# Kernel optimization log

Measured on AMD Instinct MI355X. Metric: run time of the kernel, lower is better.

## Reference

```python
import jax, jax.numpy as jnp
import numpy as np

PERIOD = 24
NUM_ITERATIONS = 2


def _window_size():
    w = max(3, PERIOD // 2)  # 12
    if w % 2 == 0:
        w += 1  # 13
    return w


def moving_average(s, w):
    # s: [N, L]; replicate-pad by w//2 on each side, then width-w mean conv ('VALID')
    pad = w // 2
    sp = jnp.pad(s, ((0, 0), (pad, pad)), mode='edge')[:, None, :]  # [N,1,L+2*pad]
    k = jnp.ones((1, 1, w), s.dtype) / w
    y = jax.lax.conv_general_dilated(sp, k, window_strides=(1,), padding='VALID',
                                     dimension_numbers=('NCH', 'OIH', 'NCH'))
    return y[:, 0, :]  # [N, L]


def extract_seasonal(d):
    # d: [N, L] with L a multiple of PERIOD. Strided indices i, i+P, ... correspond
    # to reshape [N, C, P] with fixed last axis; median over cycles, broadcast back.
    N, L = d.shape
    C = L // PERIOD
    sub = d.reshape(N, C, PERIOD)
    med = jnp.median(sub, axis=1)  # [N, P] (C=121 is odd -> matches torch.median)
    return jnp.broadcast_to(med[:, None, :], (N, C, PERIOD)).reshape(N, L)


def setup_inputs() -> dict:
    key = jax.random.key(0)
    x = jax.random.normal(key, (64, 2904, 207), dtype=jnp.float32)
    return {"x": x}


def reference(x):
    # x: [B, L, F] -> process all features at once as [B*F, L]
    B, L, F = x.shape
    s = jnp.transpose(x, (0, 2, 1)).reshape(B * F, L)
    w = _window_size()
    trend = moving_average(s, w)
    for _ in range(NUM_ITERATIONS):
        seasonal = extract_seasonal(s - trend)
        trend = moving_average(s - seasonal, w)
    residual = s - trend - seasonal

    def unflatten(a):
        return jnp.transpose(a.reshape(B, F, L), (0, 2, 1))  # [B, L, F]

    return unflatten(trend), unflatten(seasonal), unflatten(residual)
```

## Files before the change

### kernel.cpp

```cpp
#include <hip/hip_runtime.h>

#define LROW    2904
#define PERIOD  24
#define CYC     121
#define NF      207
#define NB      64
#define NROWS   13248
#define FCH     8
#define NCH     26
#define KPADW   9
#define KLDS    (PERIOD * 61 * KPADW)
#define NT      256
#define LTILE   24
#define NLT     121
#define K2GRID  (NB * NLT)
#define K2CHUNK (K2GRID / 8)
#define R13     (1.f / 13.f)

typedef unsigned short us2 __attribute__((ext_vector_type(2)));

__device__ __forceinline__ int clampi(int i) {
    return i < 0 ? 0 : (i >= LROW ? LROW - 1 : i);
}
__device__ __forceinline__ unsigned quantk(float d) {
    int ki = (int)fmaf(d, 4096.f, 32768.f);
    ki = ki < 0 ? 0 : (ki > 65535 ? 65535 : ki);
    return (unsigned)ki;
}
__device__ __forceinline__ float dqmid(unsigned k) {
    return ((float)(int)k - 32767.5f) * (1.f / 4096.f);
}

__device__ __forceinline__ unsigned selN_split(const unsigned (&K)[31], int thr) {
    unsigned T = 0;
    const us2 one2 = __builtin_bit_cast(us2, 0x00010001u);
    for (int bit = 15; bit >= 0; --bit) {
        unsigned Tp = T | (1u << bit);
        unsigned tm32 = (Tp - 1u) | ((Tp - 1u) << 16);
        us2 tm2 = __builtin_bit_cast(us2, tm32);
        us2 acc = __builtin_bit_cast(us2, 0u);
        #pragma unroll
        for (int s = 0; s < 31; ++s) {
            us2 kv = __builtin_bit_cast(us2, K[s]);
            us2 dd = __builtin_elementwise_sub_sat(kv, tm2);
            us2 mm = __builtin_elementwise_min(dd, one2);
            acc = acc + mm;
        }
        unsigned a = __builtin_bit_cast(unsigned, acc);
        int cnt = (int)(a & 0xFFFFu) + (int)(a >> 16);
        cnt += __shfl_xor(cnt, 1);
        if (cnt >= thr) T = Tp;
    }
    return T;
}

__device__ __forceinline__ void loadK31(const unsigned* keyl, int p, int f,
                                        int half, unsigned (&K)[31]) {
    const int base = p * 61 * KPADW + f;
    if (!half) {
        #pragma unroll
        for (int s = 0; s < 31; ++s) K[s] = keyl[base + s * KPADW];
    } else {
        #pragma unroll
        for (int s = 0; s < 30; ++s) K[s] = keyl[base + (31 + s) * KPADW];
        K[30] = 0u;
    }
}

__global__ __launch_bounds__(256) void k_median(const float* __restrict__ x,
                                                float* __restrict__ wsTab) {
    __shared__ unsigned keyl[KLDS];
    __shared__ unsigned short m0s[PERIOD * FCH];
    __shared__ float medBs[12 * FCH];

    const int d   = blockIdx.x;
    const int blk = (d & 7) * 208 + (d >> 3);
    const int b   = blk & 63;
    const int ch  = blk >> 6;
    const int f0  = ch * FCH;
    const int t   = threadIdx.x;

    for (int i = t; i < KLDS; i += NT) keyl[i] = 0xFFFFFFFFu;
    __syncthreads();

    {
        const int f   = t & 7;
        const int seg = t >> 3;
        const int fe  = (f0 + f < NF) ? (f0 + f) : (NF - 1);
        const float* xb = x + (size_t)b * (LROW * NF) + fe;
        const int l0 = seg * 91;
        int c = l0 / PERIOD;
        int p = l0 - c * PERIOD;
        unsigned short* k16 = (unsigned short*)keyl;

        float r[13];
        float sum = 0.f;
        #pragma unroll
        for (int i = 0; i < 13; ++i) {
            int li = l0 - 7 + i; if (li < 0) li = 0;
            r[i] = xb[(size_t)li * NF];
            sum += r[i];
        }
        #pragma unroll 13
        for (int j = 0; j < 91; ++j) {
            const int l = l0 + j;
            int la = l + 6; if (la > LROW - 1) la = LROW - 1;
            float xn = xb[(size_t)la * NF];
            sum += xn - r[0];
            unsigned k = quantk(r[7] - sum * R13);
            if (l < LROW) {
                int idx = (p * 61 + (c >> 1)) * KPADW + f;
                k16[idx * 2 + (c & 1)] = (unsigned short)k;
            }
            #pragma unroll
            for (int i = 0; i < 12; ++i) r[i] = r[i + 1];
            r[12] = xn;
            ++p; if (p == PERIOD) { p = 0; ++c; }
        }
    }
    __syncthreads();

    {
        const int sel = t >> 1, half = t & 1;
        const int f = sel & 7, p = sel >> 3;
        unsigned K[31]; loadK31(keyl, p, f, half, K);
        unsigned T = selN_split(K, 62);
        if (!half) m0s[p * FCH + f] = (unsigned short)T;
    }
    if (t < 128) {
        const int sel = t >> 1, half = t & 1;
        const int f = sel & 7, p = 16 + (sel >> 3);
        unsigned K[31]; loadK31(keyl, p, f, half, K);
        unsigned T = selN_split(K, 62);
        if (!half) m0s[p * FCH + f] = (unsigned short)T;
    }
    __syncthreads();

    if (t < 192) {
        const int sel = t >> 1, half = t & 1;
        const int f = sel & 7, e = sel >> 3;
        const int p = (e < 6) ? e : e + 12;

        float m0[PERIOD];
        #pragma unroll
        for (int q = 0; q < PERIOD; ++q)
            m0[q] = dqmid(m0s[q * FCH + f]);

        float wph = 0.f, we = 0.f;
        #pragma unroll
        for (int ee = 0; ee < 12; ++ee) if (ee == e) {
            const int pp = (ee < 6) ? ee : ee + 12;
            #pragma unroll
            for (int q = 0; q < 13; ++q) wph += m0[(pp + 18 + q) % 24];
            #pragma unroll
            for (int q = -6; q <= 6; ++q) {
                int aa = pp + q; if (aa < 0) aa = 0; if (aa > 23) aa = 23;
                we += m0[aa];
            }
        }

        unsigned K[31]; loadK31(keyl, p, f, half, K);
        unsigned m = (unsigned)m0s[p * FCH + f];
        unsigned xk = ((unsigned short*)keyl)
                      [((p * 61 + (p < 6 ? 0 : 60)) * KPADW + f) * 2];
        unsigned y = quantk(dqmid(xk) + (we - wph) * R13);

        int thr = (y > m) ? 61 : 63;
        unsigned v = selN_split(K, thr);
        bool up = (y > m) && (xk <= m);
        bool dn = (y < m) && (xk >= m);
        unsigned nm = up ? (y < v ? y : v) : (dn ? (y > v ? y : v) : m);
        if (!half) medBs[e * FCH + f] = dqmid(nm) + wph * R13;
    }
    __syncthreads();

    if (t < FCH && f0 + t < NF) {
        const int f = t;
        float m0[PERIOD];
        #pragma unroll
        for (int q = 0; q < PERIOD; ++q)
            m0[q] = dqmid(m0s[q * FCH + f]);
        float W0[PERIOD];
        {
            float s = 0.f;
            #pragma unroll
            for (int q = 0; q < 13; ++q) s += m0[q];
            W0[0] = s;
            #pragma unroll
            for (int q = 1; q < PERIOD; ++q)
                W0[q] = W0[q - 1] + m0[(q + 12) % 24] - m0[q - 1];
        }
        float lm[PERIOD];
        #pragma unroll
        for (int e = 0; e < 12; ++e) {
            int p = (e < 6) ? e : e + 12;
            lm[p] = medBs[e * FCH + f];
        }
        #pragma unroll
        for (int p = 6; p < 18; ++p) lm[p] = m0[p] + W0[p - 6] * R13;
        float wt[PERIOD];
        {
            float s = 0.f;
            #pragma unroll
            for (int q = 0; q < 13; ++q) s += lm[q];
            wt[0] = s;
            #pragma unroll
            for (int q = 1; q < PERIOD; ++q)
                wt[q] = wt[q - 1] + lm[(q + 12) % 24] - lm[q - 1];
        }
        float* wrow = wsTab + (size_t)b * 48 * NF + (f0 + f);
        #pragma unroll
        for (int i = 0; i < PERIOD; ++i) {
            wrow[(size_t)i * NF]        = lm[i];
            wrow[(size_t)(24 + i) * NF] = wt[i];
        }
    }
}

__global__ __launch_bounds__(NT, 5) void stl_outputs(const float* __restrict__ x,
                                                     const float* __restrict__ ws,
                                                     float* __restrict__ out) {
    __shared__ float T[(LTILE + 12) * NF];

    const int d   = blockIdx.x;
    const int blk = (d & 7) * K2CHUNK + (d >> 3);
    const int b  = blk / NLT;
    const int kk = blk - b * NLT;
    const int l0 = kk * LTILE;
    const int t  = threadIdx.x;
    const float* xb = x + (size_t)b * (LROW * NF);

    if (kk != 0 && kk != NLT - 1) {
        const float2* s2 = (const float2*)(xb + (size_t)(l0 - 6) * NF);
        float2* t2 = (float2*)T;
        for (int i = t; i < (LTILE + 12) * NF / 2; i += NT) t2[i] = s2[i];
    } else {
        for (int i = t; i < (LTILE + 12) * NF; i += NT) {
            int lr = i / NF;
            int ff = i - lr * NF;
            T[i] = xb[(size_t)clampi(l0 - 6 + lr) * NF + ff];
        }
    }
    __syncthreads();

    if (t < NF) {
        float lm[PERIOD], wt[PERIOD];
        const float* wrow = ws + (size_t)b * 48 * NF + t;
        #pragma unroll
        for (int i = 0; i < PERIOD; ++i) lm[i] = wrow[(size_t)i * NF];
        #pragma unroll
        for (int i = 0; i < PERIOD; ++i) wt[i] = wrow[(size_t)(PERIOD + i) * NF];

        float s13 = 0.f;
        #pragma unroll
        for (int r = 0; r < 13; ++r) s13 += T[r * NF + t];

        const bool edgeLo = (kk == 0), edgeHi = (kk == NLT - 1);
        const size_t S = (size_t)NROWS * LROW;
        const size_t obase = (size_t)b * (LROW * NF) + (size_t)l0 * NF + (size_t)t;

        #pragma unroll
        for (int j = 0; j < LTILE; ++j) {
            float W = wt[(j + 18) % 24];
            if (edgeLo && j < 6) {
                float w = 0.f;
                #pragma unroll
                for (int jj = -6; jj <= 6; ++jj) { int m = j + jj; if (m < 0) m = 0; w += lm[m]; }
                W = w;
            }
            if (edgeHi && j >= 18) {
                float w = 0.f;
                #pragma unroll
                for (int jj = -6; jj <= 6; ++jj) { int m = j + jj; if (m > 23) m = 23; w += lm[m]; }
                W = w;
            }
            float tr = (s13 - W) * R13;
            float se = lm[j];
            float re = T[(j + 6) * NF + t] - tr - se;
            size_t o = obase + (size_t)(j * NF);
            __builtin_nontemporal_store(tr, &out[o]);
            __builtin_nontemporal_store(se, &out[S + o]);
            __builtin_nontemporal_store(re, &out[2 * S + o]);
            if (j < LTILE - 1)
                s13 += T[(j + 13) * NF + t] - T[j * NF + t];
        }
    }
}

extern "C" void kernel_launch(void* const* d_in, const int* in_sizes, int n_in,
                              void* d_out, int out_size, void* d_ws, size_t ws_size,
                              hipStream_t stream) {
    const float* x = (const float*)d_in[0];
    float* out = (float*)d_out;
    float* wsTab = (float*)d_ws;
    (void)in_sizes; (void)n_in; (void)out_size; (void)ws_size;

    hipLaunchKernelGGL(k_median, dim3(NB * NCH), dim3(NT), 0, stream, x, wsTab);
    hipLaunchKernelGGL(stl_outputs, dim3(K2GRID), dim3(NT), 0, stream,
                       x, wsTab, out);
}
```

Baseline: 406.6 us.

## Stage input through LDS in chunks for the median key-building phase

Replaces the per-thread strided global loads in the sliding-window key construction with a cooperative chunked load of 376 rows × 8 features into shared memory. Threads then compute the width-13 moving average from LDS in 12-row segments. It also changes the block-to-(batch, feature-chunk) mapping, which alters the L2 access order across blocks. The aim is better load parallelism and coalescing; the cost is extra LDS (which may cut occupancy), 16 additional barriers per block and a non-unrolled inner loop.

```diff
diff --git a/kernel.cpp b/kernel.cpp
--- a/kernel.cpp
+++ b/kernel.cpp
@@ -10,6 +10,8 @@
 #define NCH     26
 #define KPADW   9
 #define KLDS    (PERIOD * 61 * KPADW)
+#define XROWS   376
+#define XSTR    9
 #define NT      256
 #define LTILE   24
 #define NLT     121
@@ -70,52 +72,56 @@
 __global__ __launch_bounds__(256) void k_median(const float* __restrict__ x,
                                                 float* __restrict__ wsTab) {
     __shared__ unsigned keyl[KLDS];
+    __shared__ float    X[XROWS * XSTR];
     __shared__ unsigned short m0s[PERIOD * FCH];
-    __shared__ float medBs[12 * FCH];
+    __shared__ float    medBs[12 * FCH];
 
     const int d   = blockIdx.x;
     const int blk = (d & 7) * 208 + (d >> 3);
-    const int b   = blk & 63;
-    const int ch  = blk >> 6;
+    const int b   = blk / NCH;
+    const int ch  = blk - b * NCH;
     const int f0  = ch * FCH;
     const int t   = threadIdx.x;
+    const float* xb = x + (size_t)b * (LROW * NF);
 
     for (int i = t; i < KLDS; i += NT) keyl[i] = 0xFFFFFFFFu;
-    __syncthreads();
-
-    {
-        const int f   = t & 7;
-        const int seg = t >> 3;
-        const int fe  = (f0 + f < NF) ? (f0 + f) : (NF - 1);
-        const float* xb = x + (size_t)b * (LROW * NF) + fe;
-        const int l0 = seg * 91;
-        int c = l0 / PERIOD;
-        int p = l0 - c * PERIOD;
-        unsigned short* k16 = (unsigned short*)keyl;
-
-        float r[13];
-        float sum = 0.f;
-        #pragma unroll
-        for (int i = 0; i < 13; ++i) {
-            int li = l0 - 7 + i; if (li < 0) li = 0;
-            r[i] = xb[(size_t)li * NF];
-            sum += r[i];
-        }
-        #pragma unroll 13
-        for (int j = 0; j < 91; ++j) {
-            const int l = l0 + j;
-            int la = l + 6; if (la > LROW - 1) la = LROW - 1;
-            float xn = xb[(size_t)la * NF];
-            sum += xn - r[0];
-            unsigned k = quantk(r[7] - sum * R13);
-            if (l < LROW) {
-                int idx = (p * 61 + (c >> 1)) * KPADW + f;
-                k16[idx * 2 + (c & 1)] = (unsigned short)k;
+
+    const int fker = t & 7;
+    const int seg  = t >> 3;
+    unsigned short* k16 = (unsigned short*)keyl;
+
+    #pragma unroll 1
+    for (int chunk = 0; chunk < 8; ++chunk) {
+        const int lc0 = chunk * 363;
+        __syncthreads();
+        for (int i = t; i < XROWS * FCH; i += NT) {
+            int lr = i >> 3, ff = i & 7;
+            int l  = clampi(lc0 - 7 + lr);
+            int fe = f0 + ff; if (fe > NF - 1) fe = NF - 1;
+            X[lr * XSTR + ff] = xb[(size_t)l * NF + fe];
+        }
+        __syncthreads();
+        {
+            const int r0 = seg * 12;
+            if (r0 < 363) {
+                const int nr = (363 - r0 < 12) ? (363 - r0) : 12;
+                int l = lc0 + r0;
+                int c = l / PERIOD;
+                int p = l - c * PERIOD;
+                float sum = 0.f;
+                #pragma unroll
+                for (int k = 1; k <= 13; ++k)
+                    sum += X[(r0 + k) * XSTR + fker];
+                #pragma unroll 1
+                for (int j = 0; j < nr; ++j) {
+                    const int r = r0 + j;
+                    unsigned kq = quantk(X[(r + 7) * XSTR + fker] - sum * R13);
+                    k16[((p * 61 + (c >> 1)) * KPADW + fker) * 2 + (c & 1)]
+                        = (unsigned short)kq;
+                    sum += X[(r + 14) * XSTR + fker] - X[(r + 1) * XSTR + fker];
+                    ++p; if (p == PERIOD) { p = 0; ++c; }
+                }
             }
-            #pragma unroll
-            for (int i = 0; i < 12; ++i) r[i] = r[i + 1];
-            r[12] = xn;
-            ++p; if (p == PERIOD) { p = 0; ++c; }
         }
     }
     __syncthreads();
```

Result: slower. 465.5 us (+14.5%).
